# Kernel optimization log

Hardware: AMD Instinct MI355X
Metric: run time of the kernel (lower is better)

The kernel has to match this reference:

```python
import jax, jax.numpy as jnp
import numpy as np


def setup_inputs() -> dict:
    key = jax.random.key(0)
    k1, k2, k3 = jax.random.split(key, 3)
    B, L, D = 8, 4096, 320
    CB_DIM, N_BOOKS = 16, 8192
    input_values = jax.random.normal(k1, (B, L, D), dtype=jnp.float32)
    # mask all ones -> static masked-select shape N = B*L
    mask_time_indices = jnp.ones((B, L), dtype=jnp.int32)
    # xavier_uniform for Linear(D -> CB_DIM, bias=False): limit = sqrt(6/(fan_in+fan_out))
    limit = float(np.sqrt(6.0 / (D + CB_DIM)))
    proj_weight = jax.random.uniform(k2, (CB_DIM, D), dtype=jnp.float32, minval=-limit, maxval=limit)
    code_book = jax.random.normal(k3, (N_BOOKS, CB_DIM), dtype=jnp.float32)
    return {"input_values": input_values, "mask_time_indices": mask_time_indices,
            "proj_weight": proj_weight, "code_book": code_book}


def reference(input_values, mask_time_indices, proj_weight, code_book):
    # input_values: [B, L, D]; mask is all-ones so masked select == flatten (static shape N=B*L)
    B, L, D = input_values.shape
    flat = input_values.reshape(B * L, D)  # [N, D]
    targets = flat @ proj_weight.T  # [N, cb_dim]  (random projection, no bias)
    # argmin over Euclidean norm == argmin over squared distance (monotone),
    # expanded form avoids the [N, n_books, cb_dim] broadcast intermediate.
    t2 = jnp.sum(targets * targets, axis=-1, keepdims=True)        # [N, 1]
    c2 = jnp.sum(code_book * code_book, axis=-1)                   # [n_books]
    d2 = t2 - 2.0 * (targets @ code_book.T) + c2                   # [N, n_books]
    labels = jnp.argmin(d2, axis=-1)                               # [N]
    return labels
```

## Files before the change

kernel.cpp:

```cpp
#include <hip/hip_runtime.h>

#define N_ROWS 32768
#define D_IN 320
#define CB 16
#define N_BOOKS 8192

typedef __attribute__((ext_vector_type(8))) short bf16x8;
typedef __attribute__((ext_vector_type(4))) float f32x4;
#define MFMA __builtin_amdgcn_mfma_f32_16x16x32_bf16
#define AS1 __attribute__((address_space(1)))
#define AS3 __attribute__((address_space(3)))

__device__ __forceinline__ unsigned short bf16rn(float f) {
  unsigned u = __float_as_uint(f);
  u += 0x7fffu + ((u >> 16) & 1u);
  return (unsigned short)(u >> 16);
}
__device__ __forceinline__ float bf16tof(unsigned short h) {
  return __uint_as_float(((unsigned)h) << 16);
}
__device__ __forceinline__ void gload_lds16(const short* g, short* l) {
  __builtin_amdgcn_global_load_lds((const AS1 unsigned int*)g, (AS3 unsigned int*)l, 16, 0, 0);
}

__global__ __launch_bounds__(256, 2) void proj_prep_kernel(
    const float* __restrict__ x, const float* __restrict__ w, short* __restrict__ tsplit,
    const float* __restrict__ cbk, short* __restrict__ bfrag, float* __restrict__ nh_g,
    int* __restrict__ ctr) {
  __shared__ __align__(16) short wfrag[3][10][64][8];
  __shared__ __align__(16) float xs[2][64 * 36];
  const int tid = threadIdx.x;

  if (blockIdx.x >= 512) {
    const int bid = blockIdx.x - 512;
    if (bid == 0 && tid == 0) *ctr = 0;
    const int j = bid * 256 + tid;
    const float4* src = (const float4*)(cbk + (size_t)j * CB);
    float4 a = src[0], b = src[1], c = src[2], d = src[3];
    float ce[16] = {a.x, a.y, a.z, a.w, b.x, b.y, b.z, b.w,
                    c.x, c.y, c.z, c.w, d.x, d.y, d.z, d.w};
    short c1[16], c2[16];
    double s = 0.0;
#pragma unroll
    for (int i = 0; i < 16; i++) {
      s += (double)ce[i] * (double)ce[i];
      unsigned short x1 = bf16rn(ce[i]);
      float r1 = ce[i] - bf16tof(x1);
      unsigned short x2 = bf16rn(r1);
      c1[i] = (short)x1; c2[i] = (short)x2;
    }
    nh_g[j] = (float)(-0.5 * s);
    bf16x8 lo1, hi1, lo2, hi2;
#pragma unroll
    for (int i = 0; i < 8; i++) {
      lo1[i] = c1[i]; hi1[i] = c1[i + 8];
      lo2[i] = c2[i]; hi2[i] = c2[i + 8];
    }
    const int bt = j >> 4, n = j & 15;
    short* base = bfrag + (size_t)bt * 1024;
    *(bf16x8*)(base + (0 * 16 + n) * 8) = lo1;
    *(bf16x8*)(base + (1 * 16 + n) * 8) = hi1;
    *(bf16x8*)(base + (2 * 16 + n) * 8) = lo1;
    *(bf16x8*)(base + (3 * 16 + n) * 8) = hi1;
    *(bf16x8*)(base + 512 + (0 * 16 + n) * 8) = lo2;
    *(bf16x8*)(base + 512 + (1 * 16 + n) * 8) = hi2;
    *(bf16x8*)(base + 512 + (2 * 16 + n) * 8) = lo2;
    *(bf16x8*)(base + 512 + (3 * 16 + n) * 8) = hi2;
    return;
  }

  const int lane = tid & 63;
  const int wv = tid >> 6;

  for (int i = tid; i < D_IN * CB; i += 256) {
    int d = i >> 4, o = i & 15;
    float f = w[o * D_IN + d];
    unsigned short h1 = bf16rn(f);
    float r1 = f - bf16tof(h1);
    unsigned short h2 = bf16rn(r1);
    float r2 = r1 - bf16tof(h2);
    unsigned short h3 = bf16rn(r2);
    int c = d >> 5, qq = (d >> 3) & 3, pos = d & 7;
    int ln = qq * 16 + o;
    wfrag[0][c][ln][pos] = (short)h1;
    wfrag[1][c][ln][pos] = (short)h2;
    wfrag[2][c][ln][pos] = (short)h3;
  }

  const float* xblk = x + (size_t)blockIdx.x * 64 * D_IN;
  {
    int row = tid >> 2, k0 = (tid & 3) * 8;
    float4 v0 = *(const float4*)(xblk + row * D_IN + k0);
    float4 v1 = *(const float4*)(xblk + row * D_IN + k0 + 4);
    *(float4*)&xs[0][row * 36 + k0] = v0;
    *(float4*)&xs[0][row * 36 + k0 + 4] = v1;
  }
  __syncthreads();

  const int m = lane & 15, q = lane >> 4;
  f32x4 g1 = {0.f, 0.f, 0.f, 0.f}, g2 = {0.f, 0.f, 0.f, 0.f}, g3 = {0.f, 0.f, 0.f, 0.f};
  for (int c = 0; c < 10; c++) {
    const int buf = c & 1;
    if (c < 9) {
      int row = tid >> 2, k0 = (tid & 3) * 8;
      float4 v0 = *(const float4*)(xblk + row * D_IN + (c + 1) * 32 + k0);
      float4 v1 = *(const float4*)(xblk + row * D_IN + (c + 1) * 32 + k0 + 4);
      *(float4*)&xs[buf ^ 1][row * 36 + k0] = v0;
      *(float4*)&xs[buf ^ 1][row * 36 + k0 + 4] = v1;
    }
    const float* xp = &xs[buf][(wv * 16 + m) * 36 + q * 8];
    float4 xa = *(const float4*)xp;
    float4 xb = *(const float4*)(xp + 4);
    float xe[8] = {xa.x, xa.y, xa.z, xa.w, xb.x, xb.y, xb.z, xb.w};
    bf16x8 a1, a2, a3;
#pragma unroll
    for (int j = 0; j < 8; j++) {
      unsigned short h1 = bf16rn(xe[j]);
      float r1 = xe[j] - bf16tof(h1);
      unsigned short h2 = bf16rn(r1);
      float r2 = r1 - bf16tof(h2);
      unsigned short h3 = bf16rn(r2);
      a1[j] = (short)h1; a2[j] = (short)h2; a3[j] = (short)h3;
    }
    bf16x8 b1 = *(const bf16x8*)wfrag[0][c][lane];
    bf16x8 b2 = *(const bf16x8*)wfrag[1][c][lane];
    bf16x8 b3 = *(const bf16x8*)wfrag[2][c][lane];
    g1 = MFMA(a1, b1, g1, 0, 0, 0);
    g2 = MFMA(a2, b1, g2, 0, 0, 0);
    g2 = MFMA(a1, b2, g2, 0, 0, 0);
    g3 = MFMA(a3, b1, g3, 0, 0, 0);
    g3 = MFMA(a1, b3, g3, 0, 0, 0);
    g3 = MFMA(a2, b2, g3, 0, 0, 0);
    __syncthreads();
  }

  float* tl = (float*)xs;
#pragma unroll
  for (int r = 0; r < 4; r++) {
    double t = (double)g1[r] + ((double)g2[r] + (double)g3[r]);
    tl[(wv * 16 + q * 4 + r) * 17 + m] = (float)t;
  }
  __syncthreads();
  {
    int row_l = tid >> 2, p = tid & 3;
    short h1[4], h2[4], h3[4];
#pragma unroll
    for (int i = 0; i < 4; i++) {
      float f = tl[row_l * 17 + p * 4 + i];
      unsigned short a = bf16rn(f);
      float r1 = f - bf16tof(a);
      unsigned short b = bf16rn(r1);
      float r2 = r1 - bf16tof(b);
      unsigned short cc = bf16rn(r2);
      h1[i] = (short)a; h2[i] = (short)b; h3[i] = (short)cc;
    }
    size_t base = (size_t)(blockIdx.x * 64 + row_l) * 48;
    *(short4*)(tsplit + base + p * 4) = make_short4(h1[0], h1[1], h1[2], h1[3]);
    *(short4*)(tsplit + base + 16 + p * 4) = make_short4(h2[0], h2[1], h2[2], h2[3]);
    *(short4*)(tsplit + base + 32 + p * 4) = make_short4(h3[0], h3[1], h3[2], h3[3]);
  }
}

#define SC_H 8

__global__ __launch_bounds__(256, 2) void score_kernel(const short* __restrict__ tsplit,
                                                       const short* __restrict__ bfrag,
                                                       const float* __restrict__ nh_g,
                                                       float4* __restrict__ cand) {
  __shared__ __align__(16) short ldsb[2][8192];
  __shared__ float ldsnh[1024];
  const int tid = threadIdx.x;
  const int lane = tid & 63;
  const int wv = tid >> 6;
  const int m = lane & 15, q = lane >> 4;
  const int rb = blockIdx.x & 127;
  const int h = blockIdx.x >> 7;
  const int rowbase = rb * 256;

  bf16x8 A12[4];
#pragma unroll
  for (int rt = 0; rt < 4; rt++) {
    int row = rowbase + wv * 64 + rt * 16 + m;
    A12[rt] = *(const bf16x8*)(tsplit + (size_t)row * 48 + q * 8);
  }
  for (int i = tid; i < 1024; i += 256) ldsnh[i] = nh_g[h * 1024 + i];

  const short* gq = bfrag + (size_t)h * 65536;
  {
    const short* g0 = gq + wv * 512 + lane * 8;
#pragma unroll
    for (int it = 0; it < 4; it++)
      gload_lds16(g0 + it * 2048, &ldsb[0][it * 2048 + wv * 512]);
  }

  const unsigned qmask = 0xFFFFFFC0u;
  float s1[4][4], s2[4][4];
#pragma unroll
  for (int rt = 0; rt < 4; rt++)
#pragma unroll
    for (int r = 0; r < 4; r++) { s1[rt][r] = -3.4e38f; s2[rt][r] = -3.4e38f; }

  __syncthreads();

  for (int sc = 0; sc < 8; sc++) {
    const int cur = sc & 1;
    if (sc < 7) {
      const short* gs = gq + (sc + 1) * 8192 + wv * 512 + lane * 8;
#pragma unroll
      for (int it = 0; it < 4; it++)
        gload_lds16(gs + it * 2048, &ldsb[cur ^ 1][it * 2048 + wv * 512]);
    }
#pragma unroll
    for (int bt = 0; bt < 8; bt++) {
      const short* bp = &ldsb[cur][bt * 1024];
      bf16x8 b1 = *(const bf16x8*)(bp + lane * 8);
      bf16x8 b2 = *(const bf16x8*)(bp + 512 + lane * 8);
      const int btg = sc * 8 + bt;
      float nh0 = ldsnh[btg * 16 + m];
      f32x4 ci = {nh0, nh0, nh0, nh0};
      const unsigned tagv = (unsigned)(63 - btg);
#pragma unroll
      for (int rt = 0; rt < 4; rt++) {
        f32x4 acc = MFMA(A12[rt], b1, ci, 0, 0, 0);
        acc = MFMA(A12[rt], b2, acc, 0, 0, 0);
#pragma unroll
        for (int r = 0; r < 4; r++) {
          float vq = __uint_as_float((__float_as_uint(acc[r]) & qmask) | tagv);
          s2[rt][r] = __builtin_amdgcn_fmed3f(vq, s1[rt][r], s2[rt][r]);
          s1[rt][r] = fmaxf(s1[rt][r], vq);
        }
      }
    }
    __syncthreads();
  }

#pragma unroll
  for (int rt = 0; rt < 4; rt++)
#pragma unroll
    for (int r = 0; r < 4; r++) {
      float s1v = s1[rt][r], s2v = s2[rt][r];
      const float ps1 = s1v;
#pragma unroll
      for (int msk = 1; msk <= 8; msk <<= 1) {
        float o1 = __shfl_xor(s1v, msk);
        float o2 = __shfl_xor(s2v, msk);
        s2v = __builtin_amdgcn_fmed3f(s1v, o1, fmaxf(s2v, o2));
        s1v = fmaxf(s1v, o1);
      }
      unsigned long long bal = __ballot(ps1 == s1v);
      unsigned grp = (unsigned)((bal >> (q * 16)) & 0xFFFFull);
      int mwin = __builtin_ctz(grp | 0x10000u);
      int btwin = 63 - (int)(__float_as_uint(s1v) & 63u);
      int col = h * 1024 + btwin * 16 + mwin;
      if (m == 0) {
        int row = rowbase + wv * 64 + rt * 16 + q * 4 + r;
        cand[(size_t)h * N_ROWS + row] = make_float4(s1v, s2v, __int_as_float(col), 0.f);
      }
    }
}

#define MARGIN_EPS 1.0e-3f

__global__ __launch_bounds__(256) void merge_flag_kernel(const float4* __restrict__ cand,
                                                         int* __restrict__ out,
                                                         int* __restrict__ list,
                                                         int* __restrict__ ctr) {
  const int r = blockIdx.x * 256 + threadIdx.x;
  float S1 = -3.4e38f, S2 = -3.4e38f;
  int I = 0;
#pragma unroll
  for (int h = 0; h < SC_H; h++) {
    float4 v = cand[(size_t)h * N_ROWS + r];
    if (v.x > S1) {
      S2 = fmaxf(S1, v.y); S1 = v.x; I = __float_as_int(v.z);
    } else {
      S2 = fmaxf(S2, v.x);
    }
  }
  out[r] = I;
  if (S1 - S2 < MARGIN_EPS) {
    int slot = atomicAdd(ctr, 1);
    list[slot] = r;
  }
}

__global__ __launch_bounds__(256) void rescore_kernel(const int* __restrict__ list,
                                                      const int* __restrict__ ctr,
                                                      const float* __restrict__ x,
                                                      const float* __restrict__ w,
                                                      const float* __restrict__ codebook,
                                                      int* __restrict__ out) {
  __shared__ double ps[16][17];
  __shared__ double tsh[16];
  __shared__ double rs[256];
  __shared__ int ri[256];
  const int tid = threadIdx.x;
  const int total = ctr[0];

  for (int it = blockIdx.x; it < total; it += gridDim.x) {
    const int row = list[it];
    {
      int o = tid & 15, c = tid >> 4;
      double p = 0.0;
      for (int k = 0; k < 20; k++) {
        int d = c * 20 + k;
        p = fma((double)x[(size_t)row * D_IN + d], (double)w[o * D_IN + d], p);
      }
      ps[c][o] = p;
    }
    __syncthreads();
    if (tid < 16) {
      double t = 0.0;
      for (int c = 0; c < 16; c++) t += ps[c][tid];
      tsh[tid] = t;
    }
    __syncthreads();
    double t[16];
#pragma unroll
    for (int i = 0; i < 16; i++) t[i] = tsh[i];
    double bs = -1.0e300;
    int bi = 0;
    for (int j = tid; j < N_BOOKS; j += 256) {
      const float* cp = codebook + (size_t)j * CB;
      double dot = 0.0, cc = 0.0;
#pragma unroll
      for (int i = 0; i < 16; i++) {
        double cv = (double)cp[i];
        dot = fma(t[i], cv, dot);
        cc = fma(cv, cv, cc);
      }
      double mv = dot - 0.5 * cc;
      if (mv > bs) { bs = mv; bi = j; }
    }
    rs[tid] = bs; ri[tid] = bi;
    __syncthreads();
    for (int s = 128; s > 0; s >>= 1) {
      if (tid < s) {
        double os = rs[tid + s]; int oi = ri[tid + s];
        if (os > rs[tid] || (os == rs[tid] && oi < ri[tid])) { rs[tid] = os; ri[tid] = oi; }
      }
      __syncthreads();
    }
    if (tid == 0) out[row] = ri[0];
    __syncthreads();
  }
}

extern "C" void kernel_launch(void* const* d_in, const int* in_sizes, int n_in,
                              void* d_out, int out_size, void* d_ws, size_t ws_size,
                              hipStream_t stream) {
  (void)in_sizes; (void)n_in; (void)out_size; (void)ws_size;
  const float* x = (const float*)d_in[0];
  const float* w = (const float*)d_in[2];
  const float* codebook = (const float*)d_in[3];

  char* ws = (char*)d_ws;
  short* tsplit = (short*)(ws);
  short* bfrag = (short*)(ws + (3 << 20));
  float* nh_g = (float*)(ws + (4 << 20));
  int* list = (int*)(ws + 4231168);
  int* ctr = (int*)(ws + 4362240);
  float4* cand = (float4*)(ws + (5 << 20));
  int* out = (int*)d_out;

  proj_prep_kernel<<<512 + N_BOOKS / 256, 256, 0, stream>>>(x, w, tsplit, codebook, bfrag,
                                                            nh_g, ctr);
  score_kernel<<<128 * SC_H, 256, 0, stream>>>(tsplit, bfrag, nh_g, cand);
  merge_flag_kernel<<<N_ROWS / 256, 256, 0, stream>>>(cand, out, list, ctr);
  rescore_kernel<<<512, 256, 0, stream>>>(list, ctr, x, w, codebook, out);
}
```

Measured before the change: 179.4 us.

## Fuse merge and rescore kernels, widen score blocks to eight waves

Merges the candidate-merge and exact-rescore kernels into one kernel that keeps its flagged-row list in shared memory. This drops a launch, the global atomic counter and its reset. The score kernel now uses 512-thread blocks, each wave owning 32 rows instead of 64, so each block has more waves to overlap the codebook-fragment loads. The cost is that rescore work now stays in the block that flagged it, so load balance suffers if flagged rows cluster, and each wave reuses each loaded B fragment across fewer rows.

```diff
diff --git a/kernel.cpp b/kernel.cpp
--- a/kernel.cpp
+++ b/kernel.cpp
@@ -25,15 +25,13 @@
 
 __global__ __launch_bounds__(256, 2) void proj_prep_kernel(
     const float* __restrict__ x, const float* __restrict__ w, short* __restrict__ tsplit,
-    const float* __restrict__ cbk, short* __restrict__ bfrag, float* __restrict__ nh_g,
-    int* __restrict__ ctr) {
+    const float* __restrict__ cbk, short* __restrict__ bfrag, float* __restrict__ nh_g) {
   __shared__ __align__(16) short wfrag[3][10][64][8];
   __shared__ __align__(16) float xs[2][64 * 36];
   const int tid = threadIdx.x;
 
   if (blockIdx.x >= 512) {
     const int bid = blockIdx.x - 512;
-    if (bid == 0 && tid == 0) *ctr = 0;
     const int j = bid * 256 + tid;
     const float4* src = (const float4*)(cbk + (size_t)j * CB);
     float4 a = src[0], b = src[1], c = src[2], d = src[3];
@@ -163,7 +161,7 @@
 
 #define SC_H 8
 
-__global__ __launch_bounds__(256, 2) void score_kernel(const short* __restrict__ tsplit,
+__global__ __launch_bounds__(512, 2) void score_kernel(const short* __restrict__ tsplit,
                                                        const short* __restrict__ bfrag,
                                                        const float* __restrict__ nh_g,
                                                        float4* __restrict__ cand) {
@@ -177,26 +175,25 @@
   const int h = blockIdx.x >> 7;
   const int rowbase = rb * 256;
 
-  bf16x8 A12[4];
-#pragma unroll
-  for (int rt = 0; rt < 4; rt++) {
-    int row = rowbase + wv * 64 + rt * 16 + m;
+  bf16x8 A12[2];
+#pragma unroll
+  for (int rt = 0; rt < 2; rt++) {
+    int row = rowbase + wv * 32 + rt * 16 + m;
     A12[rt] = *(const bf16x8*)(tsplit + (size_t)row * 48 + q * 8);
   }
-  for (int i = tid; i < 1024; i += 256) ldsnh[i] = nh_g[h * 1024 + i];
+  for (int i = tid; i < 1024; i += 512) ldsnh[i] = nh_g[h * 1024 + i];
 
   const short* gq = bfrag + (size_t)h * 65536;
   {
-    const short* g0 = gq + wv * 512 + lane * 8;
-#pragma unroll
-    for (int it = 0; it < 4; it++)
-      gload_lds16(g0 + it * 2048, &ldsb[0][it * 2048 + wv * 512]);
+    const short* g0 = gq + wv * 1024 + lane * 8;
+    gload_lds16(g0, &ldsb[0][wv * 1024]);
+    gload_lds16(g0 + 512, &ldsb[0][wv * 1024 + 512]);
   }
 
   const unsigned qmask = 0xFFFFFFC0u;
-  float s1[4][4], s2[4][4];
-#pragma unroll
-  for (int rt = 0; rt < 4; rt++)
+  float s1[2][4], s2[2][4];
+#pragma unroll
+  for (int rt = 0; rt < 2; rt++)
 #pragma unroll
     for (int r = 0; r < 4; r++) { s1[rt][r] = -3.4e38f; s2[rt][r] = -3.4e38f; }
 
@@ -205,10 +202,9 @@
   for (int sc = 0; sc < 8; sc++) {
     const int cur = sc & 1;
     if (sc < 7) {
-      const short* gs = gq + (sc + 1) * 8192 + wv * 512 + lane * 8;
-#pragma unroll
-      for (int it = 0; it < 4; it++)
-        gload_lds16(gs + it * 2048, &ldsb[cur ^ 1][it * 2048 + wv * 512]);
+      const short* gs = gq + (sc + 1) * 8192 + wv * 1024 + lane * 8;
+      gload_lds16(gs, &ldsb[cur ^ 1][wv * 1024]);
+      gload_lds16(gs + 512, &ldsb[cur ^ 1][wv * 1024 + 512]);
     }
 #pragma unroll
     for (int bt = 0; bt < 8; bt++) {
@@ -220,7 +216,7 @@
       f32x4 ci = {nh0, nh0, nh0, nh0};
       const unsigned tagv = (unsigned)(63 - btg);
 #pragma unroll
-      for (int rt = 0; rt < 4; rt++) {
+      for (int rt = 0; rt < 2; rt++) {
         f32x4 acc = MFMA(A12[rt], b1, ci, 0, 0, 0);
         acc = MFMA(A12[rt], b2, acc, 0, 0, 0);
 #pragma unroll
@@ -235,7 +231,7 @@
   }
 
 #pragma unroll
-  for (int rt = 0; rt < 4; rt++)
+  for (int rt = 0; rt < 2; rt++)
 #pragma unroll
     for (int r = 0; r < 4; r++) {
       float s1v = s1[rt][r], s2v = s2[rt][r];
@@ -253,7 +249,7 @@
       int btwin = 63 - (int)(__float_as_uint(s1v) & 63u);
       int col = h * 1024 + btwin * 16 + mwin;
       if (m == 0) {
-        int row = rowbase + wv * 64 + rt * 16 + q * 4 + r;
+        int row = rowbase + wv * 32 + rt * 16 + q * 4 + r;
         cand[(size_t)h * N_ROWS + row] = make_float4(s1v, s2v, __int_as_float(col), 0.f);
       }
     }
@@ -261,44 +257,45 @@
 
 #define MARGIN_EPS 1.0e-3f
 
-__global__ __launch_bounds__(256) void merge_flag_kernel(const float4* __restrict__ cand,
-                                                         int* __restrict__ out,
-                                                         int* __restrict__ list,
-                                                         int* __restrict__ ctr) {
-  const int r = blockIdx.x * 256 + threadIdx.x;
-  float S1 = -3.4e38f, S2 = -3.4e38f;
-  int I = 0;
-#pragma unroll
-  for (int h = 0; h < SC_H; h++) {
-    float4 v = cand[(size_t)h * N_ROWS + r];
-    if (v.x > S1) {
-      S2 = fmaxf(S1, v.y); S1 = v.x; I = __float_as_int(v.z);
-    } else {
-      S2 = fmaxf(S2, v.x);
-    }
-  }
-  out[r] = I;
-  if (S1 - S2 < MARGIN_EPS) {
-    int slot = atomicAdd(ctr, 1);
-    list[slot] = r;
-  }
-}
-
-__global__ __launch_bounds__(256) void rescore_kernel(const int* __restrict__ list,
-                                                      const int* __restrict__ ctr,
-                                                      const float* __restrict__ x,
-                                                      const float* __restrict__ w,
-                                                      const float* __restrict__ codebook,
-                                                      int* __restrict__ out) {
+__global__ __launch_bounds__(256) void merge_rescore_kernel(const float4* __restrict__ cand,
+                                                            const float* __restrict__ x,
+                                                            const float* __restrict__ w,
+                                                            const float* __restrict__ codebook,
+                                                            int* __restrict__ out) {
+  __shared__ int lcount;
+  __shared__ int llist[256];
   __shared__ double ps[16][17];
   __shared__ double tsh[16];
   __shared__ double rs[256];
   __shared__ int ri[256];
   const int tid = threadIdx.x;
-  const int total = ctr[0];
-
-  for (int it = blockIdx.x; it < total; it += gridDim.x) {
-    const int row = list[it];
+  const int base = blockIdx.x * 256;
+  if (tid == 0) lcount = 0;
+  __syncthreads();
+  {
+    const int r = base + tid;
+    float S1 = -3.4e38f, S2 = -3.4e38f;
+    int I = 0;
+#pragma unroll
+    for (int h = 0; h < SC_H; h++) {
+      float4 v = cand[(size_t)h * N_ROWS + r];
+      if (v.x > S1) {
+        S2 = fmaxf(S1, v.y); S1 = v.x; I = __float_as_int(v.z);
+      } else {
+        S2 = fmaxf(S2, v.x);
+      }
+    }
+    out[r] = I;
+    if (S1 - S2 < MARGIN_EPS) {
+      int s = atomicAdd(&lcount, 1);
+      llist[s] = r;
+    }
+  }
+  __syncthreads();
+  const int total = lcount;
+
+  for (int it = 0; it < total; it++) {
+    const int row = llist[it];
     {
       int o = tid & 15, c = tid >> 4;
       double p = 0.0;
@@ -358,14 +355,11 @@
   short* tsplit = (short*)(ws);
   short* bfrag = (short*)(ws + (3 << 20));
   float* nh_g = (float*)(ws + (4 << 20));
-  int* list = (int*)(ws + 4231168);
-  int* ctr = (int*)(ws + 4362240);
   float4* cand = (float4*)(ws + (5 << 20));
   int* out = (int*)d_out;
 
   proj_prep_kernel<<<512 + N_BOOKS / 256, 256, 0, stream>>>(x, w, tsplit, codebook, bfrag,
-                                                            nh_g, ctr);
-  score_kernel<<<128 * SC_H, 256, 0, stream>>>(tsplit, bfrag, nh_g, cand);
-  merge_flag_kernel<<<N_ROWS / 256, 256, 0, stream>>>(cand, out, list, ctr);
-  rescore_kernel<<<512, 256, 0, stream>>>(list, ctr, x, w, codebook, out);
-}
+                                                            nh_g);
+  score_kernel<<<128 * SC_H, 512, 0, stream>>>(tsplit, bfrag, nh_g, cand);
+  merge_rescore_kernel<<<N_ROWS / 256, 256, 0, stream>>>(cand, x, w, codebook, out);
+}
```

After: 193.7 us. 8.0% more time.

## Give each wave a private LDS ring for codebook tiles and drop block barriers

Applied to the files above, without the earlier changes.

The block used to share a double-buffered LDS chunk of eight codebook tiles, loaded cooperatively and guarded by a __syncthreads per chunk. Now each wave streams all 64 tiles itself into its own four-slot LDS ring, prefetching three tiles ahead and gating on explicit s_waitcnt vmcnt instead of block barriers. The MFMAs are also interleaved across the four row tiles and wrapped in s_setprio to raise issue priority. The aim is to remove barrier stalls and let waves drift independently, at the cost of four times more global/L2 load traffic per block and reliance on hand-counted vmcnt values.

```diff
diff --git a/kernel.cpp b/kernel.cpp
--- a/kernel.cpp
+++ b/kernel.cpp
@@ -167,7 +167,7 @@
                                                        const short* __restrict__ bfrag,
                                                        const float* __restrict__ nh_g,
                                                        float4* __restrict__ cand) {
-  __shared__ __align__(16) short ldsb[2][8192];
+  __shared__ __align__(16) short ldsb[4][4][1024];
   __shared__ float ldsnh[1024];
   const int tid = threadIdx.x;
   const int lane = tid & 63;
@@ -185,12 +185,12 @@
   }
   for (int i = tid; i < 1024; i += 256) ldsnh[i] = nh_g[h * 1024 + i];
 
-  const short* gq = bfrag + (size_t)h * 65536;
-  {
-    const short* g0 = gq + wv * 512 + lane * 8;
-#pragma unroll
-    for (int it = 0; it < 4; it++)
-      gload_lds16(g0 + it * 2048, &ldsb[0][it * 2048 + wv * 512]);
+  const short* gw = bfrag + (size_t)h * 65536 + lane * 8;
+  short* mybuf = &ldsb[wv][0][0];
+#pragma unroll
+  for (int t = 0; t < 3; t++) {
+    gload_lds16(gw + t * 1024, mybuf + t * 1024);
+    gload_lds16(gw + t * 1024 + 512, mybuf + t * 1024 + 512);
   }
 
   const unsigned qmask = 0xFFFFFFC0u;
@@ -202,36 +202,51 @@
 
   __syncthreads();
 
-  for (int sc = 0; sc < 8; sc++) {
-    const int cur = sc & 1;
-    if (sc < 7) {
-      const short* gs = gq + (sc + 1) * 8192 + wv * 512 + lane * 8;
-#pragma unroll
-      for (int it = 0; it < 4; it++)
-        gload_lds16(gs + it * 2048, &ldsb[cur ^ 1][it * 2048 + wv * 512]);
-    }
-#pragma unroll
-    for (int bt = 0; bt < 8; bt++) {
-      const short* bp = &ldsb[cur][bt * 1024];
-      bf16x8 b1 = *(const bf16x8*)(bp + lane * 8);
-      bf16x8 b2 = *(const bf16x8*)(bp + 512 + lane * 8);
-      const int btg = sc * 8 + bt;
-      float nh0 = ldsnh[btg * 16 + m];
-      f32x4 ci = {nh0, nh0, nh0, nh0};
-      const unsigned tagv = (unsigned)(63 - btg);
-#pragma unroll
-      for (int rt = 0; rt < 4; rt++) {
-        f32x4 acc = MFMA(A12[rt], b1, ci, 0, 0, 0);
-        acc = MFMA(A12[rt], b2, acc, 0, 0, 0);
-#pragma unroll
-        for (int r = 0; r < 4; r++) {
-          float vq = __uint_as_float((__float_as_uint(acc[r]) & qmask) | tagv);
-          s2[rt][r] = __builtin_amdgcn_fmed3f(vq, s1[rt][r], s2[rt][r]);
-          s1[rt][r] = fmaxf(s1[rt][r], vq);
-        }
-      }
-    }
-    __syncthreads();
+  for (int t = 0; t < 64; t++) {
+    if (t < 61) {
+      const short* gs = gw + (t + 3) * 1024;
+      short* ld = mybuf + ((t + 3) & 3) * 1024;
+      gload_lds16(gs, ld);
+      gload_lds16(gs + 512, ld + 512);
+      asm volatile("s_waitcnt vmcnt(6)" ::: "memory");
+    } else if (t == 61) {
+      asm volatile("s_waitcnt vmcnt(4)" ::: "memory");
+    } else if (t == 62) {
+      asm volatile("s_waitcnt vmcnt(2)" ::: "memory");
+    } else {
+      asm volatile("s_waitcnt vmcnt(0)" ::: "memory");
+    }
+    const short* bp = mybuf + (t & 3) * 1024;
+    bf16x8 b1 = *(const bf16x8*)(bp + lane * 8);
+    bf16x8 b2 = *(const bf16x8*)(bp + 512 + lane * 8);
+    float nh0 = ldsnh[t * 16 + m];
+    f32x4 ci = {nh0, nh0, nh0, nh0};
+    __builtin_amdgcn_s_setprio(1);
+    f32x4 a0 = MFMA(A12[0], b1, ci, 0, 0, 0);
+    f32x4 a1 = MFMA(A12[1], b1, ci, 0, 0, 0);
+    f32x4 a2 = MFMA(A12[2], b1, ci, 0, 0, 0);
+    f32x4 a3 = MFMA(A12[3], b1, ci, 0, 0, 0);
+    a0 = MFMA(A12[0], b2, a0, 0, 0, 0);
+    a1 = MFMA(A12[1], b2, a1, 0, 0, 0);
+    a2 = MFMA(A12[2], b2, a2, 0, 0, 0);
+    a3 = MFMA(A12[3], b2, a3, 0, 0, 0);
+    __builtin_amdgcn_s_setprio(0);
+    const unsigned tagv = (unsigned)(63 - t);
+#pragma unroll
+    for (int r = 0; r < 4; r++) {
+      float vq0 = __uint_as_float((__float_as_uint(a0[r]) & qmask) | tagv);
+      s2[0][r] = __builtin_amdgcn_fmed3f(vq0, s1[0][r], s2[0][r]);
+      s1[0][r] = fmaxf(s1[0][r], vq0);
+      float vq1 = __uint_as_float((__float_as_uint(a1[r]) & qmask) | tagv);
+      s2[1][r] = __builtin_amdgcn_fmed3f(vq1, s1[1][r], s2[1][r]);
+      s1[1][r] = fmaxf(s1[1][r], vq1);
+      float vq2 = __uint_as_float((__float_as_uint(a2[r]) & qmask) | tagv);
+      s2[2][r] = __builtin_amdgcn_fmed3f(vq2, s1[2][r], s2[2][r]);
+      s1[2][r] = fmaxf(s1[2][r], vq2);
+      float vq3 = __uint_as_float((__float_as_uint(a3[r]) & qmask) | tagv);
+      s2[3][r] = __builtin_amdgcn_fmed3f(vq3, s1[3][r], s2[3][r]);
+      s1[3][r] = fmaxf(s1[3][r], vq3);
+    }
   }
 
 #pragma unroll
```

New measurement: 192.7 us. 7.4% more time.
